# Optimization experiments

Hardware: AMD Instinct MI355X
Metric: run time of the kernel (lower is better)

## Reference

```python
import jax, jax.numpy as jnp
import numpy as np

E, K = 8, 2
B, S, H = 8, 2048, 512
R0, R1, O = 256, 256, 512
T = B * S


def _make_routing(key):
    # Mixtral-style: top-k softmax weights [T, K] and one-hot mask [E, K, T]
    k1, k2 = jax.random.split(key)
    sel = jax.random.randint(k1, (T, K), 0, E)                      # selected expert per (token, slot)
    rw = jax.nn.softmax(jax.random.normal(k2, (T, K)), axis=-1)
    mask = jax.nn.one_hot(sel, E, dtype=jnp.bool_)                  # [T, K, E]
    mask = jnp.transpose(mask, (2, 1, 0))                           # [E, K, T]
    return mask, rw


def setup_inputs() -> dict:
    key = jax.random.key(0)
    ks = jax.random.split(key, 10)
    x = jax.random.normal(ks[0], (B, S, H), dtype=jnp.float32)
    m1, rw1 = _make_routing(ks[1])
    m2, rw2 = _make_routing(ks[2])
    m3, rw3 = _make_routing(ks[3])
    s = 0.02
    W1 = jax.random.normal(ks[4], (E, R0, H), dtype=jnp.float32) * s
    b1 = jnp.zeros((E, R0), dtype=jnp.float32)
    W2 = jax.random.normal(ks[5], (E, R1, R0), dtype=jnp.float32) * s
    b2 = jnp.zeros((E, R1), dtype=jnp.float32)
    W3 = jax.random.normal(ks[6], (E, O, R1), dtype=jnp.float32) * s
    b3 = jnp.zeros((E, O), dtype=jnp.float32)
    return {"x": x,
            "expert_mask1": m1, "expert_mask2": m2, "expert_mask3": m3,
            "routing_weights1": rw1, "routing_weights2": rw2, "routing_weights3": rw3,
            "W1": W1, "b1": b1, "W2": W2, "b2": b2, "W3": W3, "b3": b3}


def _moe_stage(h, mask, rw, W, b, act):
    # combine[e, t] = routing weight of token t for expert e (0 if not routed)
    cmb = jnp.einsum('ekt,tk->et', mask.astype(h.dtype), rw)
    acc0 = jnp.zeros((h.shape[0], W.shape[1]), dtype=h.dtype)

    def body(acc, ew):
        Wi, bi, ci = ew            # Wi: [out, in], bi: [out], ci: [T]
        out = h @ Wi.T + bi
        if act:
            out = jax.nn.relu(out)
        return acc + ci[:, None] * out, None

    acc, _ = jax.lax.scan(body, acc0, (W, b, cmb))
    return acc


def reference(x, expert_mask1, expert_mask2, expert_mask3,
              routing_weights1, routing_weights2, routing_weights3,
              W1, b1, W2, b2, W3, b3):
    bsz, seq, dim = x.shape
    h = x.reshape(-1, dim)                                          # [T, H]
    h = _moe_stage(h, expert_mask1, routing_weights1, W1, b1, act=False)   # [T, R0]
    h = _moe_stage(h, expert_mask2, routing_weights2, W2, b2, act=False)   # [T, R1]
    h = _moe_stage(h, expert_mask3, routing_weights3, W3, b3, act=True)    # relu on expert output, then combine
    out = jax.nn.relu(h.reshape(bsz, seq, -1))
    return out
```

## Files before the change

kernel.cpp:

```cpp
#include <hip/hip_runtime.h>

#define T_TOKENS 16384
#define CAP 12288
#define RB 48
#define CNT_STRIDE 16

typedef unsigned short u16;
typedef unsigned int u32;
typedef __attribute__((ext_vector_type(8))) short short8;
typedef __attribute__((ext_vector_type(4))) float float4v;

typedef __attribute__((address_space(1))) u32 gas_u32;
typedef __attribute__((address_space(3))) u32 las_u32;

__device__ __forceinline__ u16 f2b(float f) {
  unsigned u = __float_as_uint(f);
  u = (u + 0x7fffu + ((u >> 16) & 1u)) >> 16;
  return (u16)u;
}
__device__ __forceinline__ float b2f(u16 h) {
  return __uint_as_float(((unsigned)h) << 16);
}
__device__ __forceinline__ void gload16(const u16* g, u16* l) {
  __builtin_amdgcn_global_load_lds((gas_u32*)g, (las_u32*)l, 16, 0, 0);
}

__global__ void prep_kernel(const float* __restrict__ W1, const float* __restrict__ W2,
                            const float* __restrict__ W3,
                            const int* __restrict__ m1, const int* __restrict__ m2,
                            const int* __restrict__ m3, const float* __restrict__ rw1,
                            const float* __restrict__ rw2, const float* __restrict__ rw3,
                            u16* __restrict__ Wb1, u16* __restrict__ Wb2, u16* __restrict__ Wb3,
                            int* __restrict__ cnt, int* __restrict__ idxbuf,
                            float* __restrict__ wgtbuf) {
  __shared__ int lcnt[24];
  __shared__ int lbase[24];
  const int tid = threadIdx.x;

  if (blockIdx.x >= 64) {
    const int n1 = 8 * 256 * 512, n2 = 8 * 256 * 256;
    int base = (blockIdx.x - 64) * 2048 + tid * 8;
    const float* src;
    u16* dst;
    int off = base;
    if (base < n1) { src = W1; dst = Wb1; }
    else if (base < n1 + n2) { src = W2; dst = Wb2; off = base - n1; }
    else { src = W3; dst = Wb3; off = base - n1 - n2; }
    float4 a0 = *(const float4*)(src + off);
    float4 a1 = *(const float4*)(src + off + 4);
    short8 v;
    v[0] = (short)f2b(a0.x); v[1] = (short)f2b(a0.y);
    v[2] = (short)f2b(a0.z); v[3] = (short)f2b(a0.w);
    v[4] = (short)f2b(a1.x); v[5] = (short)f2b(a1.y);
    v[6] = (short)f2b(a1.z); v[7] = (short)f2b(a1.w);
    *(short8*)(dst + off) = v;
    return;
  }

  const int t = blockIdx.x * 256 + tid;
  if (tid < 24) lcnt[tid] = 0;
  __syncthreads();

  const int* masks[3] = {m1, m2, m3};
  const float* rws[3] = {rw1, rw2, rw3};
  int expert[3][2], lpos[3][2];
#pragma unroll
  for (int s = 0; s < 3; ++s)
#pragma unroll
    for (int k = 0; k < 2; ++k) {
      int e = 0;
#pragma unroll
      for (int j = 0; j < 8; ++j)
        if (masks[s][(j * 2 + k) * T_TOKENS + t] != 0) e = j;
      expert[s][k] = e;
      lpos[s][k] = atomicAdd(&lcnt[s * 8 + e], 1);
    }
  __syncthreads();
  if (tid < 24) lbase[tid] = atomicAdd(&cnt[tid * CNT_STRIDE], lcnt[tid]);
  __syncthreads();
#pragma unroll
  for (int s = 0; s < 3; ++s)
#pragma unroll
    for (int k = 0; k < 2; ++k) {
      int e = expert[s][k];
      int p = lbase[s * 8 + e] + lpos[s][k];
      if (p < CAP) {
        idxbuf[(s * 8 + e) * CAP + p] = t * 2 + k;
        wgtbuf[(s * 8 + e) * CAP + p] = rws[s][t * 2 + k];
      }
    }
}

template <int KDIM, int NDIM_TOTAL, int SRC, int RELU>
__global__ __launch_bounds__(512, 2) void moe_gemm(
    const void* __restrict__ Asrc, const u16* __restrict__ Wb, const float* __restrict__ bias,
    const int* __restrict__ cnt, const int* __restrict__ idxbuf, const float* __restrict__ wgtbuf,
    u16* __restrict__ outTmp) {
  __shared__ __align__(16) u16 As[128 * 64];
  __shared__ __align__(16) u16 Bs[256 * 64];
  __shared__ int rowTok[128];
  __shared__ float rowW[128];

  const int e = blockIdx.y;
  const int n_e = cnt[e * CNT_STRIDE];
  const int row0 = blockIdx.x * 128;
  if (row0 >= n_e) return;
  const int nbase = blockIdx.z * 256;
  const int tid = threadIdx.x;

  if (tid < 128) {
    int g = row0 + tid;
    if (g < n_e) {
      rowTok[tid] = idxbuf[e * CAP + g];
      rowW[tid] = wgtbuf[e * CAP + g];
    } else {
      rowTok[tid] = 0;
      rowW[tid] = 0.f;
    }
  }
  __syncthreads();

  const int wid = tid >> 6, lane = tid & 63;
  const int wr = wid >> 2, wc = wid & 3;
  const int lrow = lane & 15, lquad = lane >> 4;
  const int srow = lane >> 3;
  const int gswl = (lane & 7) ^ srow;

  const u16* Wbe = Wb + ((size_t)e * NDIM_TOTAL + nbase) * KDIM;
  const u16* bP = Wbe + (size_t)(wid * 32 + srow) * KDIM + gswl * 8;
  u16* bD = Bs + (wid * 4) * 512;

  const int arow = tid >> 3;
  const int gsrc = tid & 7;

  float4v acc[4][4];
#pragma unroll
  for (int i = 0; i < 4; ++i)
#pragma unroll
    for (int j = 0; j < 4; ++j) acc[i][j] = (float4v)0.f;

  for (int kb = 0; kb < KDIM; kb += 64) {
#pragma unroll
    for (int i = 0; i < 4; ++i)
      gload16(bP + (size_t)i * 8 * KDIM + kb, bD + i * 512);
#pragma unroll
    for (int it = 0; it < 2; ++it) {
      int r = arow + it * 64;
      int tok = rowTok[r];
      int slot = gsrc ^ (r & 7);
      short8 v;
      if (SRC == 0) {
        const float* xp = (const float*)Asrc + (size_t)(tok >> 1) * KDIM + kb + gsrc * 8;
        float4 a0 = *(const float4*)xp;
        float4 a1 = *(const float4*)(xp + 4);
        v[0] = (short)f2b(a0.x); v[1] = (short)f2b(a0.y);
        v[2] = (short)f2b(a0.z); v[3] = (short)f2b(a0.w);
        v[4] = (short)f2b(a1.x); v[5] = (short)f2b(a1.y);
        v[6] = (short)f2b(a1.z); v[7] = (short)f2b(a1.w);
      } else {
        const u16* p0 = (const u16*)Asrc + ((size_t)(tok >> 1) * 2) * KDIM + kb + gsrc * 8;
        short8 v0 = *(const short8*)p0;
        short8 v1 = *(const short8*)(p0 + KDIM);
#pragma unroll
        for (int j = 0; j < 8; ++j)
          v[j] = (short)f2b(b2f((u16)v0[j]) + b2f((u16)v1[j]));
      }
      *(short8*)&As[r * 64 + slot * 8] = v;
    }
    __syncthreads();
#pragma unroll
    for (int ks = 0; ks < 64; ks += 32) {
      const int gq = ((ks >> 3) + lquad) ^ (lrow & 7);
      short8 af[4], bfr[4];
#pragma unroll
      for (int mt = 0; mt < 4; ++mt)
        af[mt] = *(const short8*)&As[(wr * 64 + mt * 16 + lrow) * 64 + gq * 8];
#pragma unroll
      for (int nt = 0; nt < 4; ++nt)
        bfr[nt] = *(const short8*)&Bs[(wc * 64 + nt * 16 + lrow) * 64 + gq * 8];
#pragma unroll
      for (int mt = 0; mt < 4; ++mt)
#pragma unroll
        for (int nt = 0; nt < 4; ++nt)
          acc[mt][nt] = __builtin_amdgcn_mfma_f32_16x16x32_bf16(af[mt], bfr[nt], acc[mt][nt], 0, 0, 0);
    }
    __syncthreads();
  }

  float bv[4];
#pragma unroll
  for (int nt = 0; nt < 4; ++nt)
    bv[nt] = bias[e * NDIM_TOTAL + nbase + wc * 64 + nt * 16 + lrow];
#pragma unroll
  for (int mt = 0; mt < 4; ++mt) {
#pragma unroll
    for (int i = 0; i < 4; ++i) {
      int m = wr * 64 + mt * 16 + lquad * 4 + i;
      if (row0 + m < n_e) {
        float w = rowW[m];
        size_t drow = (size_t)rowTok[m] * NDIM_TOTAL + nbase;
#pragma unroll
        for (int nt = 0; nt < 4; ++nt) {
          float v = acc[mt][nt][i] + bv[nt];
          if (RELU) v = fmaxf(v, 0.f);
          v *= w;
          outTmp[drow + wc * 64 + nt * 16 + lrow] = f2b(v);
        }
      }
    }
  }
}

__global__ void finalize_kernel(const u16* __restrict__ tmp3, float* __restrict__ out) {
  int f = (blockIdx.x * 256 + threadIdx.x) * 8;
  int t = f >> 9;
  int o = f & 511;
  const u16* p = tmp3 + (size_t)t * 1024 + o;
  short8 v0 = *(const short8*)p;
  short8 v1 = *(const short8*)(p + 512);
  float4 r0, r1;
  r0.x = fmaxf(b2f((u16)v0[0]) + b2f((u16)v1[0]), 0.f);
  r0.y = fmaxf(b2f((u16)v0[1]) + b2f((u16)v1[1]), 0.f);
  r0.z = fmaxf(b2f((u16)v0[2]) + b2f((u16)v1[2]), 0.f);
  r0.w = fmaxf(b2f((u16)v0[3]) + b2f((u16)v1[3]), 0.f);
  r1.x = fmaxf(b2f((u16)v0[4]) + b2f((u16)v1[4]), 0.f);
  r1.y = fmaxf(b2f((u16)v0[5]) + b2f((u16)v1[5]), 0.f);
  r1.z = fmaxf(b2f((u16)v0[6]) + b2f((u16)v1[6]), 0.f);
  r1.w = fmaxf(b2f((u16)v0[7]) + b2f((u16)v1[7]), 0.f);
  *(float4*)(out + f) = r0;
  *(float4*)(out + f + 4) = r1;
}

extern "C" void kernel_launch(void* const* d_in, const int* in_sizes, int n_in,
                              void* d_out, int out_size, void* d_ws, size_t ws_size,
                              hipStream_t stream) {
  const float* x  = (const float*)d_in[0];
  const int* m1   = (const int*)d_in[1];
  const int* m2   = (const int*)d_in[2];
  const int* m3   = (const int*)d_in[3];
  const float* rw1 = (const float*)d_in[4];
  const float* rw2 = (const float*)d_in[5];
  const float* rw3 = (const float*)d_in[6];
  const float* W1 = (const float*)d_in[7];
  const float* b1 = (const float*)d_in[8];
  const float* W2 = (const float*)d_in[9];
  const float* b2 = (const float*)d_in[10];
  const float* W3 = (const float*)d_in[11];
  const float* b3 = (const float*)d_in[12];
  float* out = (float*)d_out;

  char* ws = (char*)d_ws;
  size_t off = 0;
  int* cnt = (int*)(ws + off); off += 24 * CNT_STRIDE * 4;
  u16* Wb1 = (u16*)(ws + off); off += (size_t)8 * 256 * 512 * 2;
  u16* Wb2 = (u16*)(ws + off); off += (size_t)8 * 256 * 256 * 2;
  u16* Wb3 = (u16*)(ws + off); off += (size_t)8 * 512 * 256 * 2;
  u16* tmp1 = (u16*)(ws + off); off += (size_t)T_TOKENS * 2 * 256 * 2;
  u16* tmp2 = (u16*)(ws + off); off += (size_t)T_TOKENS * 2 * 256 * 2;
  u16* tmp3 = (u16*)(ws + off); off += (size_t)T_TOKENS * 2 * 512 * 2;
  int* idxb = (int*)(ws + off); off += (size_t)3 * 8 * CAP * 4;
  float* wgtb = (float*)(ws + off); off += (size_t)3 * 8 * CAP * 4;

  hipMemsetAsync(cnt, 0, 24 * CNT_STRIDE * 4, stream);
  prep_kernel<<<1344, 256, 0, stream>>>(W1, W2, W3, m1, m2, m3, rw1, rw2, rw3,
                                        Wb1, Wb2, Wb3, cnt, idxb, wgtb);

  moe_gemm<512, 256, 0, 0><<<dim3(RB, 8, 1), 512, 0, stream>>>(
      x, Wb1, b1, cnt + 0, idxb + 0, wgtb + 0, tmp1);
  moe_gemm<256, 256, 1, 0><<<dim3(RB, 8, 1), 512, 0, stream>>>(
      tmp1, Wb2, b2, cnt + 8 * CNT_STRIDE, idxb + 8 * CAP, wgtb + 8 * CAP, tmp2);
  moe_gemm<256, 512, 1, 1><<<dim3(RB, 8, 2), 512, 0, stream>>>(
      tmp2, Wb3, b3, cnt + 16 * CNT_STRIDE, idxb + 16 * CAP, wgtb + 16 * CAP, tmp3);

  finalize_kernel<<<4096, 256, 0, stream>>>(tmp3, out);
}
```

Before: 187.9 us.

## Fuse all MoE stages into one persistent kernel with grid barriers

Replaces the prep kernel, three expert GEMM launches and the finalize kernel with a single persistent kernel of 256 blocks. Stages are separated by atomic spin grid barriers, and tiles are distributed round-robin across blocks. This removes per-launch overhead and the inter-kernel gaps. In exchange it depends on all 256 blocks being co-resident, and each stage now waits on a grid-wide barrier and a fixed tile schedule instead of hardware block scheduling.

```diff
diff --git a/kernel.cpp b/kernel.cpp
--- a/kernel.cpp
+++ b/kernel.cpp
@@ -4,6 +4,8 @@
 #define CAP 12288
 #define RB 48
 #define CNT_STRIDE 16
+#define NBLK 256
+#define NTHR 512
 
 typedef unsigned short u16;
 typedef unsigned int u32;
@@ -25,94 +27,37 @@
   __builtin_amdgcn_global_load_lds((gas_u32*)g, (las_u32*)l, 16, 0, 0);
 }
 
-__global__ void prep_kernel(const float* __restrict__ W1, const float* __restrict__ W2,
-                            const float* __restrict__ W3,
-                            const int* __restrict__ m1, const int* __restrict__ m2,
-                            const int* __restrict__ m3, const float* __restrict__ rw1,
-                            const float* __restrict__ rw2, const float* __restrict__ rw3,
-                            u16* __restrict__ Wb1, u16* __restrict__ Wb2, u16* __restrict__ Wb3,
-                            int* __restrict__ cnt, int* __restrict__ idxbuf,
-                            float* __restrict__ wgtbuf) {
-  __shared__ int lcnt[24];
-  __shared__ int lbase[24];
+__device__ __forceinline__ void grid_barrier(int* bars, int idx) {
+  __syncthreads();
+  if (threadIdx.x == 0) {
+    __threadfence();
+    __hip_atomic_fetch_add(&bars[idx * 16], 1, __ATOMIC_ACQ_REL, __HIP_MEMORY_SCOPE_AGENT);
+    long spins = 0;
+    while (__hip_atomic_load(&bars[idx * 16], __ATOMIC_ACQUIRE, __HIP_MEMORY_SCOPE_AGENT) < NBLK &&
+           ++spins < 400000000L) {
+      __builtin_amdgcn_s_sleep(8);
+    }
+    __threadfence();
+  }
+  __syncthreads();
+}
+
+template <int KDIM, int NDIM_TOTAL, int SRC, int RELU>
+__device__ __forceinline__ void gemm_tile(
+    const void* __restrict__ Asrc, const u16* __restrict__ Wb, const float* __restrict__ bias,
+    const int* __restrict__ cnt_s, const int* __restrict__ idx_s, const float* __restrict__ wgt_s,
+    u16* __restrict__ outTmp, int e, int row0, int nbase,
+    u16 (&As)[128 * 64], u16 (&Bs)[256 * 64], int (&rowTok)[128], float (&rowW)[128]) {
+  const int n_e = cnt_s[e * CNT_STRIDE];
+  if (row0 >= n_e) return;
   const int tid = threadIdx.x;
 
-  if (blockIdx.x >= 64) {
-    const int n1 = 8 * 256 * 512, n2 = 8 * 256 * 256;
-    int base = (blockIdx.x - 64) * 2048 + tid * 8;
-    const float* src;
-    u16* dst;
-    int off = base;
-    if (base < n1) { src = W1; dst = Wb1; }
-    else if (base < n1 + n2) { src = W2; dst = Wb2; off = base - n1; }
-    else { src = W3; dst = Wb3; off = base - n1 - n2; }
-    float4 a0 = *(const float4*)(src + off);
-    float4 a1 = *(const float4*)(src + off + 4);
-    short8 v;
-    v[0] = (short)f2b(a0.x); v[1] = (short)f2b(a0.y);
-    v[2] = (short)f2b(a0.z); v[3] = (short)f2b(a0.w);
-    v[4] = (short)f2b(a1.x); v[5] = (short)f2b(a1.y);
-    v[6] = (short)f2b(a1.z); v[7] = (short)f2b(a1.w);
-    *(short8*)(dst + off) = v;
-    return;
-  }
-
-  const int t = blockIdx.x * 256 + tid;
-  if (tid < 24) lcnt[tid] = 0;
   __syncthreads();
-
-  const int* masks[3] = {m1, m2, m3};
-  const float* rws[3] = {rw1, rw2, rw3};
-  int expert[3][2], lpos[3][2];
-#pragma unroll
-  for (int s = 0; s < 3; ++s)
-#pragma unroll
-    for (int k = 0; k < 2; ++k) {
-      int e = 0;
-#pragma unroll
-      for (int j = 0; j < 8; ++j)
-        if (masks[s][(j * 2 + k) * T_TOKENS + t] != 0) e = j;
-      expert[s][k] = e;
-      lpos[s][k] = atomicAdd(&lcnt[s * 8 + e], 1);
-    }
-  __syncthreads();
-  if (tid < 24) lbase[tid] = atomicAdd(&cnt[tid * CNT_STRIDE], lcnt[tid]);
-  __syncthreads();
-#pragma unroll
-  for (int s = 0; s < 3; ++s)
-#pragma unroll
-    for (int k = 0; k < 2; ++k) {
-      int e = expert[s][k];
-      int p = lbase[s * 8 + e] + lpos[s][k];
-      if (p < CAP) {
-        idxbuf[(s * 8 + e) * CAP + p] = t * 2 + k;
-        wgtbuf[(s * 8 + e) * CAP + p] = rws[s][t * 2 + k];
-      }
-    }
-}
-
-template <int KDIM, int NDIM_TOTAL, int SRC, int RELU>
-__global__ __launch_bounds__(512, 2) void moe_gemm(
-    const void* __restrict__ Asrc, const u16* __restrict__ Wb, const float* __restrict__ bias,
-    const int* __restrict__ cnt, const int* __restrict__ idxbuf, const float* __restrict__ wgtbuf,
-    u16* __restrict__ outTmp) {
-  __shared__ __align__(16) u16 As[128 * 64];
-  __shared__ __align__(16) u16 Bs[256 * 64];
-  __shared__ int rowTok[128];
-  __shared__ float rowW[128];
-
-  const int e = blockIdx.y;
-  const int n_e = cnt[e * CNT_STRIDE];
-  const int row0 = blockIdx.x * 128;
-  if (row0 >= n_e) return;
-  const int nbase = blockIdx.z * 256;
-  const int tid = threadIdx.x;
-
   if (tid < 128) {
     int g = row0 + tid;
     if (g < n_e) {
-      rowTok[tid] = idxbuf[e * CAP + g];
-      rowW[tid] = wgtbuf[e * CAP + g];
+      rowTok[tid] = idx_s[e * CAP + g];
+      rowW[tid] = wgt_s[e * CAP + g];
     } else {
       rowTok[tid] = 0;
       rowW[tid] = 0.f;
@@ -128,7 +73,7 @@
 
   const u16* Wbe = Wb + ((size_t)e * NDIM_TOTAL + nbase) * KDIM;
   const u16* bP = Wbe + (size_t)(wid * 32 + srow) * KDIM + gswl * 8;
-  u16* bD = Bs + (wid * 4) * 512;
+  u16* bD = &Bs[(wid * 4) * 512];
 
   const int arow = tid >> 3;
   const int gsrc = tid & 7;
@@ -211,24 +156,117 @@
   }
 }
 
-__global__ void finalize_kernel(const u16* __restrict__ tmp3, float* __restrict__ out) {
-  int f = (blockIdx.x * 256 + threadIdx.x) * 8;
-  int t = f >> 9;
-  int o = f & 511;
-  const u16* p = tmp3 + (size_t)t * 1024 + o;
-  short8 v0 = *(const short8*)p;
-  short8 v1 = *(const short8*)(p + 512);
-  float4 r0, r1;
-  r0.x = fmaxf(b2f((u16)v0[0]) + b2f((u16)v1[0]), 0.f);
-  r0.y = fmaxf(b2f((u16)v0[1]) + b2f((u16)v1[1]), 0.f);
-  r0.z = fmaxf(b2f((u16)v0[2]) + b2f((u16)v1[2]), 0.f);
-  r0.w = fmaxf(b2f((u16)v0[3]) + b2f((u16)v1[3]), 0.f);
-  r1.x = fmaxf(b2f((u16)v0[4]) + b2f((u16)v1[4]), 0.f);
-  r1.y = fmaxf(b2f((u16)v0[5]) + b2f((u16)v1[5]), 0.f);
-  r1.z = fmaxf(b2f((u16)v0[6]) + b2f((u16)v1[6]), 0.f);
-  r1.w = fmaxf(b2f((u16)v0[7]) + b2f((u16)v1[7]), 0.f);
-  *(float4*)(out + f) = r0;
-  *(float4*)(out + f + 4) = r1;
+__global__ __launch_bounds__(NTHR, 2) void moe_mega(
+    const float* __restrict__ x, const int* __restrict__ m1, const int* __restrict__ m2,
+    const int* __restrict__ m3, const float* __restrict__ rw1, const float* __restrict__ rw2,
+    const float* __restrict__ rw3, const float* __restrict__ W1, const float* __restrict__ W2,
+    const float* __restrict__ W3, const float* __restrict__ b1, const float* __restrict__ b2,
+    const float* __restrict__ b3, u16* __restrict__ Wb1, u16* __restrict__ Wb2,
+    u16* __restrict__ Wb3, u16* __restrict__ tmp1, u16* __restrict__ tmp2,
+    u16* __restrict__ tmp3, int* __restrict__ cnt, int* __restrict__ bars,
+    int* __restrict__ idxb, float* __restrict__ wgtb, float* __restrict__ out) {
+  __shared__ __align__(16) u16 As[128 * 64];
+  __shared__ __align__(16) u16 Bs[256 * 64];
+  __shared__ int rowTok[128];
+  __shared__ float rowW[128];
+  __shared__ int lcnt[24];
+  __shared__ int lbase[24];
+
+  const int tid = threadIdx.x;
+  const int blk = blockIdx.x;
+
+  if (blk < 32) {
+    const int t = blk * 512 + tid;
+    if (tid < 24) lcnt[tid] = 0;
+    __syncthreads();
+    const int* masks[3] = {m1, m2, m3};
+    const float* rws[3] = {rw1, rw2, rw3};
+    int expert[3][2], lpos[3][2];
+#pragma unroll
+    for (int s = 0; s < 3; ++s)
+#pragma unroll
+      for (int k = 0; k < 2; ++k) {
+        int e = 0;
+#pragma unroll
+        for (int j = 0; j < 8; ++j)
+          if (masks[s][(j * 2 + k) * T_TOKENS + t] != 0) e = j;
+        expert[s][k] = e;
+        lpos[s][k] = atomicAdd(&lcnt[s * 8 + e], 1);
+      }
+    __syncthreads();
+    if (tid < 24) lbase[tid] = atomicAdd(&cnt[tid * CNT_STRIDE], lcnt[tid]);
+    __syncthreads();
+#pragma unroll
+    for (int s = 0; s < 3; ++s)
+#pragma unroll
+      for (int k = 0; k < 2; ++k) {
+        int e = expert[s][k];
+        int p = lbase[s * 8 + e] + lpos[s][k];
+        if (p < CAP) {
+          idxb[(s * 8 + e) * CAP + p] = t * 2 + k;
+          wgtb[(s * 8 + e) * CAP + p] = rws[s][t * 2 + k];
+        }
+      }
+  } else {
+    const int n1 = 8 * 256 * 512, n2 = 8 * 256 * 256;
+    const int ngran = (n1 + n2 + 8 * 512 * 256) / 8;
+    for (int g = (blk - 32) * NTHR + tid; g < ngran; g += 224 * NTHR) {
+      int base = g * 8;
+      const float* src;
+      u16* dst;
+      int off = base;
+      if (base < n1) { src = W1; dst = Wb1; }
+      else if (base < n1 + n2) { src = W2; dst = Wb2; off = base - n1; }
+      else { src = W3; dst = Wb3; off = base - n1 - n2; }
+      float4 a0 = *(const float4*)(src + off);
+      float4 a1 = *(const float4*)(src + off + 4);
+      short8 v;
+      v[0] = (short)f2b(a0.x); v[1] = (short)f2b(a0.y);
+      v[2] = (short)f2b(a0.z); v[3] = (short)f2b(a0.w);
+      v[4] = (short)f2b(a1.x); v[5] = (short)f2b(a1.y);
+      v[6] = (short)f2b(a1.z); v[7] = (short)f2b(a1.w);
+      *(short8*)(dst + off) = v;
+    }
+  }
+  grid_barrier(bars, 0);
+
+  for (int tau = blk; tau < 8 * RB; tau += NBLK)
+    gemm_tile<512, 256, 0, 0>(x, Wb1, b1, cnt, idxb, wgtb, tmp1,
+                              tau & 7, (tau >> 3) * 128, 0, As, Bs, rowTok, rowW);
+  grid_barrier(bars, 1);
+
+  for (int tau = blk; tau < 8 * RB; tau += NBLK)
+    gemm_tile<256, 256, 1, 0>(tmp1, Wb2, b2, cnt + 8 * CNT_STRIDE, idxb + 8 * CAP,
+                              wgtb + 8 * CAP, tmp2,
+                              tau & 7, (tau >> 3) * 128, 0, As, Bs, rowTok, rowW);
+  grid_barrier(bars, 2);
+
+  for (int tau = blk; tau < 8 * RB * 2; tau += NBLK)
+    gemm_tile<256, 512, 1, 1>(tmp2, Wb3, b3, cnt + 16 * CNT_STRIDE, idxb + 16 * CAP,
+                              wgtb + 16 * CAP, tmp3,
+                              tau & 7, (tau >> 4) * 128, ((tau >> 3) & 1) * 256,
+                              As, Bs, rowTok, rowW);
+  grid_barrier(bars, 3);
+
+  for (int g = blk * NTHR + tid; g < (T_TOKENS * 512) / 8; g += NBLK * NTHR) {
+    int f = g * 8;
+    int t = f >> 9;
+    int o = f & 511;
+    const u16* p = tmp3 + (size_t)t * 1024 + o;
+    short8 v0 = *(const short8*)p;
+    short8 v1 = *(const short8*)(p + 512);
+    float4 r0, r1;
+    r0.x = fmaxf(b2f((u16)v0[0]) + b2f((u16)v1[0]), 0.f);
+    r0.y = fmaxf(b2f((u16)v0[1]) + b2f((u16)v1[1]), 0.f);
+    r0.z = fmaxf(b2f((u16)v0[2]) + b2f((u16)v1[2]), 0.f);
+    r0.w = fmaxf(b2f((u16)v0[3]) + b2f((u16)v1[3]), 0.f);
+    r1.x = fmaxf(b2f((u16)v0[4]) + b2f((u16)v1[4]), 0.f);
+    r1.y = fmaxf(b2f((u16)v0[5]) + b2f((u16)v1[5]), 0.f);
+    r1.z = fmaxf(b2f((u16)v0[6]) + b2f((u16)v1[6]), 0.f);
+    r1.w = fmaxf(b2f((u16)v0[7]) + b2f((u16)v1[7]), 0.f);
+    *(float4*)(out + f) = r0;
+    *(float4*)(out + f + 4) = r1;
+  }
 }
 
 extern "C" void kernel_launch(void* const* d_in, const int* in_sizes, int n_in,
@@ -252,6 +290,7 @@
   char* ws = (char*)d_ws;
   size_t off = 0;
   int* cnt = (int*)(ws + off); off += 24 * CNT_STRIDE * 4;
+  int* bars = (int*)(ws + off); off += 8 * 16 * 4;
   u16* Wb1 = (u16*)(ws + off); off += (size_t)8 * 256 * 512 * 2;
   u16* Wb2 = (u16*)(ws + off); off += (size_t)8 * 256 * 256 * 2;
   u16* Wb3 = (u16*)(ws + off); off += (size_t)8 * 512 * 256 * 2;
@@ -261,16 +300,8 @@
   int* idxb = (int*)(ws + off); off += (size_t)3 * 8 * CAP * 4;
   float* wgtb = (float*)(ws + off); off += (size_t)3 * 8 * CAP * 4;
 
-  hipMemsetAsync(cnt, 0, 24 * CNT_STRIDE * 4, stream);
-  prep_kernel<<<1344, 256, 0, stream>>>(W1, W2, W3, m1, m2, m3, rw1, rw2, rw3,
-                                        Wb1, Wb2, Wb3, cnt, idxb, wgtb);
-
-  moe_gemm<512, 256, 0, 0><<<dim3(RB, 8, 1), 512, 0, stream>>>(
-      x, Wb1, b1, cnt + 0, idxb + 0, wgtb + 0, tmp1);
-  moe_gemm<256, 256, 1, 0><<<dim3(RB, 8, 1), 512, 0, stream>>>(
-      tmp1, Wb2, b2, cnt + 8 * CNT_STRIDE, idxb + 8 * CAP, wgtb + 8 * CAP, tmp2);
-  moe_gemm<256, 512, 1, 1><<<dim3(RB, 8, 2), 512, 0, stream>>>(
-      tmp2, Wb3, b3, cnt + 16 * CNT_STRIDE, idxb + 16 * CAP, wgtb + 16 * CAP, tmp3);
-
-  finalize_kernel<<<4096, 256, 0, stream>>>(tmp3, out);
-}
+  hipMemsetAsync(cnt, 0, (24 * CNT_STRIDE + 8 * 16) * 4, stream);
+  moe_mega<<<NBLK, NTHR, 0, stream>>>(x, m1, m2, m3, rw1, rw2, rw3, W1, W2, W3,
+                                      b1, b2, b3, Wb1, Wb2, Wb3, tmp1, tmp2, tmp3,
+                                      cnt, bars, idxb, wgtb, out);
+}
```

Result: slower. 425.2 us (+126.2%).

## Double-buffer A and B tiles in LDS to overlap loads with MFMA

Applied to the files above, without the earlier changes.

Splits the LDS A and B tiles into two buffers. While the current tile is multiplied, the next K-tile's B is loaded asynchronously and A is fetched into registers, then converted and written into the alternate buffer. This hides global load latency behind compute and removes one barrier per iteration. In exchange LDS use roughly doubles to about 98KB per block, which may limit the two blocks per CU set by launch_bounds, and register pressure rises.

```diff
diff --git a/kernel.cpp b/kernel.cpp
--- a/kernel.cpp
+++ b/kernel.cpp
@@ -96,8 +96,8 @@
     const void* __restrict__ Asrc, const u16* __restrict__ Wb, const float* __restrict__ bias,
     const int* __restrict__ cnt, const int* __restrict__ idxbuf, const float* __restrict__ wgtbuf,
     u16* __restrict__ outTmp) {
-  __shared__ __align__(16) u16 As[128 * 64];
-  __shared__ __align__(16) u16 Bs[256 * 64];
+  __shared__ __align__(16) u16 As[2][128 * 64];
+  __shared__ __align__(16) u16 Bs[2][256 * 64];
   __shared__ int rowTok[128];
   __shared__ float rowW[128];
 
@@ -128,10 +128,69 @@
 
   const u16* Wbe = Wb + ((size_t)e * NDIM_TOTAL + nbase) * KDIM;
   const u16* bP = Wbe + (size_t)(wid * 32 + srow) * KDIM + gswl * 8;
-  u16* bD = Bs + (wid * 4) * 512;
 
   const int arow = tid >> 3;
   const int gsrc = tid & 7;
+  const int slotA = gsrc ^ (arow & 7);
+  const int tok0 = rowTok[arow], tok1 = rowTok[arow + 64];
+
+  const float* xr0 = nullptr; const float* xr1 = nullptr;
+  const u16* pr0 = nullptr; const u16* pr1 = nullptr;
+  if constexpr (SRC == 0) {
+    xr0 = (const float*)Asrc + (size_t)(tok0 >> 1) * KDIM + gsrc * 8;
+    xr1 = (const float*)Asrc + (size_t)(tok1 >> 1) * KDIM + gsrc * 8;
+  } else {
+    pr0 = (const u16*)Asrc + ((size_t)(tok0 >> 1) * 2) * KDIM + gsrc * 8;
+    pr1 = (const u16*)Asrc + ((size_t)(tok1 >> 1) * 2) * KDIM + gsrc * 8;
+  }
+
+  float4 f00, f01, f10, f11;
+  short8 s00, s01, s10, s11;
+
+#define STAGEB(buf_, kb_)                                                  \
+  {                                                                        \
+    _Pragma("unroll")                                                      \
+    for (int i_ = 0; i_ < 4; ++i_)                                         \
+      gload16(bP + (size_t)i_ * 8 * KDIM + (kb_), &Bs[(buf_)][(wid * 4 + i_) * 512]); \
+  }
+
+#define LOADA(kb_)                                                         \
+  {                                                                        \
+    if constexpr (SRC == 0) {                                              \
+      f00 = *(const float4*)(xr0 + (kb_));                                 \
+      f01 = *(const float4*)(xr0 + (kb_) + 4);                             \
+      f10 = *(const float4*)(xr1 + (kb_));                                 \
+      f11 = *(const float4*)(xr1 + (kb_) + 4);                             \
+    } else {                                                               \
+      s00 = *(const short8*)(pr0 + (kb_));                                 \
+      s01 = *(const short8*)(pr0 + KDIM + (kb_));                          \
+      s10 = *(const short8*)(pr1 + (kb_));                                 \
+      s11 = *(const short8*)(pr1 + KDIM + (kb_));                          \
+    }                                                                      \
+  }
+
+#define WRITEA(buf_)                                                       \
+  {                                                                        \
+    short8 v0_, v1_;                                                       \
+    if constexpr (SRC == 0) {                                              \
+      v0_[0] = (short)f2b(f00.x); v0_[1] = (short)f2b(f00.y);              \
+      v0_[2] = (short)f2b(f00.z); v0_[3] = (short)f2b(f00.w);              \
+      v0_[4] = (short)f2b(f01.x); v0_[5] = (short)f2b(f01.y);              \
+      v0_[6] = (short)f2b(f01.z); v0_[7] = (short)f2b(f01.w);              \
+      v1_[0] = (short)f2b(f10.x); v1_[1] = (short)f2b(f10.y);              \
+      v1_[2] = (short)f2b(f10.z); v1_[3] = (short)f2b(f10.w);              \
+      v1_[4] = (short)f2b(f11.x); v1_[5] = (short)f2b(f11.y);              \
+      v1_[6] = (short)f2b(f11.z); v1_[7] = (short)f2b(f11.w);              \
+    } else {                                                               \
+      _Pragma("unroll")                                                    \
+      for (int j_ = 0; j_ < 8; ++j_) {                                     \
+        v0_[j_] = (short)f2b(b2f((u16)s00[j_]) + b2f((u16)s01[j_]));       \
+        v1_[j_] = (short)f2b(b2f((u16)s10[j_]) + b2f((u16)s11[j_]));       \
+      }                                                                    \
+    }                                                                      \
+    *(short8*)&As[(buf_)][arow * 64 + slotA * 8] = v0_;                    \
+    *(short8*)&As[(buf_)][(arow + 64) * 64 + slotA * 8] = v1_;             \
+  }
 
   float4v acc[4][4];
 #pragma unroll
@@ -139,53 +198,42 @@
 #pragma unroll
     for (int j = 0; j < 4; ++j) acc[i][j] = (float4v)0.f;
 
+  STAGEB(0, 0);
+  LOADA(0);
+  WRITEA(0);
+  __syncthreads();
+
+  int cur = 0;
   for (int kb = 0; kb < KDIM; kb += 64) {
-#pragma unroll
-    for (int i = 0; i < 4; ++i)
-      gload16(bP + (size_t)i * 8 * KDIM + kb, bD + i * 512);
-#pragma unroll
-    for (int it = 0; it < 2; ++it) {
-      int r = arow + it * 64;
-      int tok = rowTok[r];
-      int slot = gsrc ^ (r & 7);
-      short8 v;
-      if (SRC == 0) {
-        const float* xp = (const float*)Asrc + (size_t)(tok >> 1) * KDIM + kb + gsrc * 8;
-        float4 a0 = *(const float4*)xp;
-        float4 a1 = *(const float4*)(xp + 4);
-        v[0] = (short)f2b(a0.x); v[1] = (short)f2b(a0.y);
-        v[2] = (short)f2b(a0.z); v[3] = (short)f2b(a0.w);
-        v[4] = (short)f2b(a1.x); v[5] = (short)f2b(a1.y);
-        v[6] = (short)f2b(a1.z); v[7] = (short)f2b(a1.w);
-      } else {
-        const u16* p0 = (const u16*)Asrc + ((size_t)(tok >> 1) * 2) * KDIM + kb + gsrc * 8;
-        short8 v0 = *(const short8*)p0;
-        short8 v1 = *(const short8*)(p0 + KDIM);
-#pragma unroll
-        for (int j = 0; j < 8; ++j)
-          v[j] = (short)f2b(b2f((u16)v0[j]) + b2f((u16)v1[j]));
-      }
-      *(short8*)&As[r * 64 + slot * 8] = v;
-    }
-    __syncthreads();
+    const int nxt = kb + 64;
+    if (nxt < KDIM) {
+      STAGEB(cur ^ 1, nxt);
+      LOADA(nxt);
+    }
 #pragma unroll
     for (int ks = 0; ks < 64; ks += 32) {
       const int gq = ((ks >> 3) + lquad) ^ (lrow & 7);
       short8 af[4], bfr[4];
 #pragma unroll
       for (int mt = 0; mt < 4; ++mt)
-        af[mt] = *(const short8*)&As[(wr * 64 + mt * 16 + lrow) * 64 + gq * 8];
+        af[mt] = *(const short8*)&As[cur][(wr * 64 + mt * 16 + lrow) * 64 + gq * 8];
 #pragma unroll
       for (int nt = 0; nt < 4; ++nt)
-        bfr[nt] = *(const short8*)&Bs[(wc * 64 + nt * 16 + lrow) * 64 + gq * 8];
+        bfr[nt] = *(const short8*)&Bs[cur][(wc * 64 + nt * 16 + lrow) * 64 + gq * 8];
 #pragma unroll
       for (int mt = 0; mt < 4; ++mt)
 #pragma unroll
         for (int nt = 0; nt < 4; ++nt)
           acc[mt][nt] = __builtin_amdgcn_mfma_f32_16x16x32_bf16(af[mt], bfr[nt], acc[mt][nt], 0, 0, 0);
     }
+    if (nxt < KDIM) WRITEA(cur ^ 1);
     __syncthreads();
-  }
+    cur ^= 1;
+  }
+
+#undef STAGEB
+#undef LOADA
+#undef WRITEA
 
   float bv[4];
 #pragma unroll
```

New measurement: 210.1 us. 1.12x slower.

## Double-buffer weight tiles, prefetch activations in registers, pre-convert x to bf16

Applied to the files above, without the earlier changes.

The GEMM main loop now double-buffers the B (weight) tile in LDS and prefetches the next A rows into registers while the MFMAs run on the current tile. This is meant to overlap global loads with compute. x is converted to bf16 once in the prep kernel rather than inside each stage-1 GEMM block. Row token indices are kept in registers and re-read from global memory in the epilogue, which drops the LDS tables and one barrier. Launch bounds move to 4 blocks per CU, which may cause register pressure or spills. The larger LDS footprint from double buffering may also cap occupancy.

```diff
diff --git a/kernel.cpp b/kernel.cpp
--- a/kernel.cpp
+++ b/kernel.cpp
@@ -26,11 +26,12 @@
 }
 
 __global__ void prep_kernel(const float* __restrict__ W1, const float* __restrict__ W2,
-                            const float* __restrict__ W3,
+                            const float* __restrict__ W3, const float* __restrict__ x,
                             const int* __restrict__ m1, const int* __restrict__ m2,
                             const int* __restrict__ m3, const float* __restrict__ rw1,
                             const float* __restrict__ rw2, const float* __restrict__ rw3,
                             u16* __restrict__ Wb1, u16* __restrict__ Wb2, u16* __restrict__ Wb3,
+                            u16* __restrict__ xb,
                             int* __restrict__ cnt, int* __restrict__ idxbuf,
                             float* __restrict__ wgtbuf) {
   __shared__ int lcnt[24];
@@ -38,14 +39,15 @@
   const int tid = threadIdx.x;
 
   if (blockIdx.x >= 64) {
-    const int n1 = 8 * 256 * 512, n2 = 8 * 256 * 256;
+    const int n1 = 8 * 256 * 512, n2 = 8 * 256 * 256, n3 = 8 * 512 * 256;
     int base = (blockIdx.x - 64) * 2048 + tid * 8;
     const float* src;
     u16* dst;
     int off = base;
     if (base < n1) { src = W1; dst = Wb1; }
     else if (base < n1 + n2) { src = W2; dst = Wb2; off = base - n1; }
-    else { src = W3; dst = Wb3; off = base - n1 - n2; }
+    else if (base < n1 + n2 + n3) { src = W3; dst = Wb3; off = base - n1 - n2; }
+    else { src = x; dst = xb; off = base - n1 - n2 - n3; }
     float4 a0 = *(const float4*)(src + off);
     float4 a1 = *(const float4*)(src + off + 4);
     short8 v;
@@ -92,14 +94,12 @@
 }
 
 template <int KDIM, int NDIM_TOTAL, int SRC, int RELU>
-__global__ __launch_bounds__(512, 2) void moe_gemm(
-    const void* __restrict__ Asrc, const u16* __restrict__ Wb, const float* __restrict__ bias,
+__global__ __launch_bounds__(512, 4) void moe_gemm(
+    const u16* __restrict__ Asrc, const u16* __restrict__ Wb, const float* __restrict__ bias,
     const int* __restrict__ cnt, const int* __restrict__ idxbuf, const float* __restrict__ wgtbuf,
     u16* __restrict__ outTmp) {
   __shared__ __align__(16) u16 As[128 * 64];
-  __shared__ __align__(16) u16 Bs[256 * 64];
-  __shared__ int rowTok[128];
-  __shared__ float rowW[128];
+  __shared__ __align__(16) u16 Bs[2][256 * 64];
 
   const int e = blockIdx.y;
   const int n_e = cnt[e * CNT_STRIDE];
@@ -108,18 +108,6 @@
   const int nbase = blockIdx.z * 256;
   const int tid = threadIdx.x;
 
-  if (tid < 128) {
-    int g = row0 + tid;
-    if (g < n_e) {
-      rowTok[tid] = idxbuf[e * CAP + g];
-      rowW[tid] = wgtbuf[e * CAP + g];
-    } else {
-      rowTok[tid] = 0;
-      rowW[tid] = 0.f;
-    }
-  }
-  __syncthreads();
-
   const int wid = tid >> 6, lane = tid & 63;
   const int wr = wid >> 2, wc = wid & 3;
   const int lrow = lane & 15, lquad = lane >> 4;
@@ -128,10 +116,56 @@
 
   const u16* Wbe = Wb + ((size_t)e * NDIM_TOTAL + nbase) * KDIM;
   const u16* bP = Wbe + (size_t)(wid * 32 + srow) * KDIM + gswl * 8;
-  u16* bD = Bs + (wid * 4) * 512;
 
   const int arow = tid >> 3;
   const int gsrc = tid & 7;
+  const int slotA = gsrc ^ (arow & 7);
+  const int g0 = row0 + arow, g1 = row0 + arow + 64;
+  const int tok0 = (g0 < n_e) ? idxbuf[e * CAP + g0] : 0;
+  const int tok1 = (g1 < n_e) ? idxbuf[e * CAP + g1] : 0;
+
+  const u16* pr0;
+  const u16* pr1;
+  if constexpr (SRC == 0) {
+    pr0 = Asrc + (size_t)(tok0 >> 1) * KDIM + gsrc * 8;
+    pr1 = Asrc + (size_t)(tok1 >> 1) * KDIM + gsrc * 8;
+  } else {
+    pr0 = Asrc + ((size_t)(tok0 >> 1) * 2) * KDIM + gsrc * 8;
+    pr1 = Asrc + ((size_t)(tok1 >> 1) * 2) * KDIM + gsrc * 8;
+  }
+
+  short8 s00, s01, s10, s11;
+
+#define STAGEB(buf_, kb_)                                                       \
+  {                                                                             \
+    _Pragma("unroll")                                                           \
+    for (int i_ = 0; i_ < 4; ++i_)                                              \
+      gload16(bP + (size_t)i_ * 8 * KDIM + (kb_), &Bs[(buf_)][(wid * 4 + i_) * 512]); \
+  }
+
+#define LOADA(kb_)                                                              \
+  {                                                                             \
+    s00 = *(const short8*)(pr0 + (kb_));                                        \
+    s10 = *(const short8*)(pr1 + (kb_));                                        \
+    if constexpr (SRC == 1) {                                                   \
+      s01 = *(const short8*)(pr0 + KDIM + (kb_));                               \
+      s11 = *(const short8*)(pr1 + KDIM + (kb_));                               \
+    }                                                                           \
+  }
+
+#define WRITEA()                                                                \
+  {                                                                             \
+    short8 v0_ = s00, v1_ = s10;                                                \
+    if constexpr (SRC == 1) {                                                   \
+      _Pragma("unroll")                                                         \
+      for (int j_ = 0; j_ < 8; ++j_) {                                          \
+        v0_[j_] = (short)f2b(b2f((u16)s00[j_]) + b2f((u16)s01[j_]));            \
+        v1_[j_] = (short)f2b(b2f((u16)s10[j_]) + b2f((u16)s11[j_]));            \
+      }                                                                         \
+    }                                                                           \
+    *(short8*)&As[arow * 64 + slotA * 8] = v0_;                                 \
+    *(short8*)&As[(arow + 64) * 64 + slotA * 8] = v1_;                          \
+  }
 
   float4v acc[4][4];
 #pragma unroll
@@ -139,35 +173,18 @@
 #pragma unroll
     for (int j = 0; j < 4; ++j) acc[i][j] = (float4v)0.f;
 
-  for (int kb = 0; kb < KDIM; kb += 64) {
-#pragma unroll
-    for (int i = 0; i < 4; ++i)
-      gload16(bP + (size_t)i * 8 * KDIM + kb, bD + i * 512);
-#pragma unroll
-    for (int it = 0; it < 2; ++it) {
-      int r = arow + it * 64;
-      int tok = rowTok[r];
-      int slot = gsrc ^ (r & 7);
-      short8 v;
-      if (SRC == 0) {
-        const float* xp = (const float*)Asrc + (size_t)(tok >> 1) * KDIM + kb + gsrc * 8;
-        float4 a0 = *(const float4*)xp;
-        float4 a1 = *(const float4*)(xp + 4);
-        v[0] = (short)f2b(a0.x); v[1] = (short)f2b(a0.y);
-        v[2] = (short)f2b(a0.z); v[3] = (short)f2b(a0.w);
-        v[4] = (short)f2b(a1.x); v[5] = (short)f2b(a1.y);
-        v[6] = (short)f2b(a1.z); v[7] = (short)f2b(a1.w);
-      } else {
-        const u16* p0 = (const u16*)Asrc + ((size_t)(tok >> 1) * 2) * KDIM + kb + gsrc * 8;
-        short8 v0 = *(const short8*)p0;
-        short8 v1 = *(const short8*)(p0 + KDIM);
-#pragma unroll
-        for (int j = 0; j < 8; ++j)
-          v[j] = (short)f2b(b2f((u16)v0[j]) + b2f((u16)v1[j]));
-      }
-      *(short8*)&As[r * 64 + slot * 8] = v;
-    }
-    __syncthreads();
+  STAGEB(0, 0);
+  LOADA(0);
+  WRITEA();
+  __syncthreads();
+
+  int buf = 0;
+  for (int kb = 0;;) {
+    const int nxt = kb + 64;
+    if (nxt < KDIM) {
+      STAGEB(buf ^ 1, nxt);
+      LOADA(nxt);
+    }
 #pragma unroll
     for (int ks = 0; ks < 64; ks += 32) {
       const int gq = ((ks >> 3) + lquad) ^ (lrow & 7);
@@ -177,15 +194,24 @@
         af[mt] = *(const short8*)&As[(wr * 64 + mt * 16 + lrow) * 64 + gq * 8];
 #pragma unroll
       for (int nt = 0; nt < 4; ++nt)
-        bfr[nt] = *(const short8*)&Bs[(wc * 64 + nt * 16 + lrow) * 64 + gq * 8];
+        bfr[nt] = *(const short8*)&Bs[buf][(wc * 64 + nt * 16 + lrow) * 64 + gq * 8];
 #pragma unroll
       for (int mt = 0; mt < 4; ++mt)
 #pragma unroll
         for (int nt = 0; nt < 4; ++nt)
           acc[mt][nt] = __builtin_amdgcn_mfma_f32_16x16x32_bf16(af[mt], bfr[nt], acc[mt][nt], 0, 0, 0);
     }
+    if (nxt >= KDIM) break;
     __syncthreads();
-  }
+    WRITEA();
+    __syncthreads();
+    buf ^= 1;
+    kb = nxt;
+  }
+
+#undef STAGEB
+#undef LOADA
+#undef WRITEA
 
   float bv[4];
 #pragma unroll
@@ -196,9 +222,10 @@
 #pragma unroll
     for (int i = 0; i < 4; ++i) {
       int m = wr * 64 + mt * 16 + lquad * 4 + i;
-      if (row0 + m < n_e) {
-        float w = rowW[m];
-        size_t drow = (size_t)rowTok[m] * NDIM_TOTAL + nbase;
+      int g = row0 + m;
+      if (g < n_e) {
+        float w = wgtbuf[e * CAP + g];
+        size_t drow = (size_t)idxbuf[e * CAP + g] * NDIM_TOTAL + nbase;
 #pragma unroll
         for (int nt = 0; nt < 4; ++nt) {
           float v = acc[mt][nt][i] + bv[nt];
@@ -255,6 +282,7 @@
   u16* Wb1 = (u16*)(ws + off); off += (size_t)8 * 256 * 512 * 2;
   u16* Wb2 = (u16*)(ws + off); off += (size_t)8 * 256 * 256 * 2;
   u16* Wb3 = (u16*)(ws + off); off += (size_t)8 * 512 * 256 * 2;
+  u16* xb  = (u16*)(ws + off); off += (size_t)T_TOKENS * 512 * 2;
   u16* tmp1 = (u16*)(ws + off); off += (size_t)T_TOKENS * 2 * 256 * 2;
   u16* tmp2 = (u16*)(ws + off); off += (size_t)T_TOKENS * 2 * 256 * 2;
   u16* tmp3 = (u16*)(ws + off); off += (size_t)T_TOKENS * 2 * 512 * 2;
@@ -262,11 +290,11 @@
   float* wgtb = (float*)(ws + off); off += (size_t)3 * 8 * CAP * 4;
 
   hipMemsetAsync(cnt, 0, 24 * CNT_STRIDE * 4, stream);
-  prep_kernel<<<1344, 256, 0, stream>>>(W1, W2, W3, m1, m2, m3, rw1, rw2, rw3,
-                                        Wb1, Wb2, Wb3, cnt, idxb, wgtb);
+  prep_kernel<<<5440, 256, 0, stream>>>(W1, W2, W3, x, m1, m2, m3, rw1, rw2, rw3,
+                                        Wb1, Wb2, Wb3, xb, cnt, idxb, wgtb);
 
   moe_gemm<512, 256, 0, 0><<<dim3(RB, 8, 1), 512, 0, stream>>>(
-      x, Wb1, b1, cnt + 0, idxb + 0, wgtb + 0, tmp1);
+      xb, Wb1, b1, cnt + 0, idxb + 0, wgtb + 0, tmp1);
   moe_gemm<256, 256, 1, 0><<<dim3(RB, 8, 1), 512, 0, stream>>>(
       tmp1, Wb2, b2, cnt + 8 * CNT_STRIDE, idxb + 8 * CAP, wgtb + 8 * CAP, tmp2);
   moe_gemm<256, 512, 1, 1><<<dim3(RB, 8, 2), 512, 0, stream>>>(
```

New measurement: 221.4 us. 1.18x slower.
